# Kernel tuning notes

Hardware: AMD Instinct MI355X
Metric: run time of the kernel (lower is better)

Reference implementation:

```python
import jax, jax.numpy as jnp
import numpy as np

NUM_HEADS = 32  # head_dim = input_dim // num_heads = 32 == C (forced by matmul contraction)


def setup_inputs() -> dict:
    key = jax.random.key(0)
    ks = jax.random.split(key, 8)
    B, C, D3, H1 = 16, 32, 1, 32
    input_dim = 1024  # == C**2, forced by the final view(B, C, H1, W1)
    s = 0.02
    x1 = jax.random.normal(ks[0], (B, C, D3, H1, input_dim), jnp.float32)
    x2 = jax.random.normal(ks[1], (B, C, D3, H1, input_dim), jnp.float32)
    Wq = jax.random.normal(ks[2], (input_dim, input_dim), jnp.float32) * s
    bq = jax.random.normal(ks[3], (input_dim,), jnp.float32) * s
    Wk = jax.random.normal(ks[4], (input_dim, input_dim), jnp.float32) * s
    bk = jax.random.normal(ks[5], (input_dim,), jnp.float32) * s
    Wv = jax.random.normal(ks[6], (input_dim, input_dim), jnp.float32) * s
    bv = jax.random.normal(ks[7], (input_dim,), jnp.float32) * s
    return {"x1": x1, "x2": x2, "Wq": Wq, "bq": bq, "Wk": Wk, "bk": bk, "Wv": Wv, "bv": bv}


def reference(x1, x2, Wq, bq, Wk, bk, Wv, bv):
    B, C, _, H1, W1 = x1.shape  # W1 == input_dim (Linear acts on last dim)
    nh = NUM_HEADS
    hd = W1 // nh
    # Linear projections on the last axis (torch Linear: x @ W.T + b)
    q = (x1 @ Wq.T + bq).reshape(B, C, nh, hd, -1).transpose(0, 2, 4, 3, 1)  # (B, nh, L1, hd, C)
    k = (x2 @ Wk.T + bk).reshape(B, C, nh, hd, -1)                            # (B, C, nh, hd, L2)
    v = (x2 @ Wv.T + bv).reshape(B, C, nh, hd, -1)                            # (B, C, nh, hd, L2)
    # Broadcasted batched matmul: contracts q's trailing C axis with k's hd axis (C == hd).
    energy = jnp.matmul(q, k)                      # (B, C, L1, hd, L2)
    attention = jax.nn.softmax(energy, axis=-1)    # softmax over L2
    # Contracts v's L2 axis with attention's hd axis (L2 == hd).
    out = jnp.matmul(v, attention)                 # (B, C, L1, hd, L2)
    out = out.transpose(0, 2, 4, 3, 1).reshape(B, C, H1, W1)
    return out
```

## Files before the change

kernel.cpp:

```cpp
#include <hip/hip_runtime.h>
#include <cstdint>

typedef __bf16 bf16x8 __attribute__((ext_vector_type(8)));
typedef float f32x4 __attribute__((ext_vector_type(4)));
typedef unsigned short us8 __attribute__((ext_vector_type(8)));

__device__ __forceinline__ unsigned short f2bf(float f) {
  union { float f; uint32_t u; } c; c.f = f;
  uint32_t u = c.u + 0x7FFFu + ((c.u >> 16) & 1u);
  return (unsigned short)(u >> 16);
}

__global__ __launch_bounds__(256) void cvt5(
    const float* __restrict__ x1, const float* __restrict__ x2,
    const float* __restrict__ Wq, const float* __restrict__ Wk, const float* __restrict__ Wv,
    unsigned short* __restrict__ xb1, unsigned short* __restrict__ xb2,
    unsigned short* __restrict__ wb) {
  int z = blockIdx.y;
  const float* src; unsigned short* dst; int n4;
  if (z == 0)      { src = x1; dst = xb1;            n4 = 16777216 / 4; }
  else if (z == 1) { src = x2; dst = xb2;            n4 = 16777216 / 4; }
  else if (z == 2) { src = Wq; dst = wb;             n4 = 1048576 / 4; }
  else if (z == 3) { src = Wk; dst = wb + 1048576;   n4 = 1048576 / 4; }
  else             { src = Wv; dst = wb + 2*1048576; n4 = 1048576 / 4; }
  for (int i = blockIdx.x * 256 + threadIdx.x; i < n4; i += gridDim.x * 256) {
    float4 v = ((const float4*)src)[i];
    ushort4 o;
    o.x = f2bf(v.x); o.y = f2bf(v.y); o.z = f2bf(v.z); o.w = f2bf(v.w);
    ((ushort4*)dst)[i] = o;
  }
}

__device__ __forceinline__ void stage_half(const unsigned short* __restrict__ g,
                                           unsigned short* l, int wv, int rl, int cg) {
#pragma unroll
  for (int ld = 0; ld < 2; ++ld) {
    const int chunk = wv * 2 + ld;
    const unsigned short* gp = g + (chunk * 8 + rl) * 1024 + cg * 8;
    unsigned short* lp = l + chunk * 512;
    __builtin_amdgcn_global_load_lds((const __attribute__((address_space(1))) void*)gp,
                                     (__attribute__((address_space(3))) void*)lp,
                                     16, 0, 0);
  }
}

__global__ __launch_bounds__(512) void gemm_qkv(
    const unsigned short* __restrict__ xb1, const unsigned short* __restrict__ xb2,
    const unsigned short* __restrict__ wb,
    const float* __restrict__ bq, const float* __restrict__ bk, const float* __restrict__ bv,
    unsigned short* __restrict__ qkv) {
  __shared__ __attribute__((aligned(16))) unsigned short sm[65536];
  unsigned short* lA0 = sm;
  unsigned short* lB0 = sm + 16384;
  unsigned short* lA1 = sm + 32768;
  unsigned short* lB1 = sm + 49152;

  const int id = blockIdx.x;
  const int swz = (id & 7) * 96 + (id >> 3);
  const int z = swz >> 8;
  const int rem = swz & 255;
  const int mb = rem >> 2;
  const int nb = rem & 3;
  const int m0 = mb * 256;
  const int n0 = nb * 256;

  const unsigned short* Ag = (z == 0) ? xb1 : xb2;
  const unsigned short* Wg = wb + z * 1048576;
  const float* bias = (z == 0) ? bq : (z == 1 ? bk : bv);
  unsigned short* C = qkv + z * 16777216;

  const int tid = threadIdx.x;
  const int lane = tid & 63;
  const int wv = tid >> 6;
  const int wm = wv >> 2;
  const int wn = wv & 3;
  const int mr = lane & 15;
  const int quad = lane >> 4;

  const int rl = lane >> 3;
  const int cg = (lane & 7) ^ rl;

  const int sg0 = ((quad) ^ (mr & 7)) * 8;
  const int sg1 = ((4 + quad) ^ (mr & 7)) * 8;
  const int arow = (wm * 128 + mr) * 64;
  const int brow = (wn * 64 + mr) * 64;

  f32x4 acc[8][4];
#pragma unroll
  for (int i = 0; i < 8; ++i)
#pragma unroll
    for (int j = 0; j < 4; ++j) acc[i][j] = (f32x4){0.f, 0.f, 0.f, 0.f};

  bf16x8 af[4][2], bfr[4][2];

  auto STA = [&](unsigned short* dst, int kt) {
    const unsigned short* g = Ag + m0 * 1024 + kt * 64;
    stage_half(g, dst, wv, rl, cg);
    stage_half(g + 128 * 1024, dst + 8192, wv, rl, cg);
  };
  auto STB = [&](unsigned short* dst, int kt) {
    const unsigned short* g = Wg + n0 * 1024 + kt * 64;
    stage_half(g, dst, wv, rl, cg);
    stage_half(g + 128 * 1024, dst + 8192, wv, rl, cg);
  };
  auto RDA = [&](const unsigned short* lA, int ib) {
#pragma unroll
    for (int i = 0; i < 4; ++i) {
      af[i][0] = *(const bf16x8*)(lA + arow + (ib + i) * 1024 + sg0);
      af[i][1] = *(const bf16x8*)(lA + arow + (ib + i) * 1024 + sg1);
    }
  };
  auto RDB = [&](const unsigned short* lB, int jb) {
#pragma unroll
    for (int j = 0; j < 2; ++j) {
      bfr[jb + j][0] = *(const bf16x8*)(lB + brow + (jb + j) * 1024 + sg0);
      bfr[jb + j][1] = *(const bf16x8*)(lB + brow + (jb + j) * 1024 + sg1);
    }
  };
  auto MF = [&](int ib, int jb) {
#pragma unroll
    for (int i = 0; i < 4; ++i)
#pragma unroll
      for (int j = 0; j < 2; ++j)
#pragma unroll
        for (int h = 0; h < 2; ++h)
          acc[ib + i][jb + j] = __builtin_amdgcn_mfma_f32_16x16x32_bf16(
              af[i][h], bfr[jb + j][h], acc[ib + i][jb + j], 0, 0, 0);
  };

  STA(lA0, 0);
  STB(lB0, 0);
  STA(lA1, 1);
  asm volatile("s_waitcnt vmcnt(4)" ::: "memory");
  __builtin_amdgcn_s_barrier();

#pragma unroll 1
  for (int t = 0; t < 8; ++t) {
    const bool lastt = (t == 7);
    RDA(lA0, 0); RDB(lB0, 0);
    STB(lB1, 2 * t + 1);
    __builtin_amdgcn_s_barrier();
    __builtin_amdgcn_s_setprio(1); MF(0, 0); __builtin_amdgcn_s_setprio(0);
    __builtin_amdgcn_s_barrier();
    RDB(lB0, 2);
    __builtin_amdgcn_s_barrier();
    __builtin_amdgcn_s_setprio(1); MF(0, 2); __builtin_amdgcn_s_setprio(0);
    __builtin_amdgcn_s_barrier();
    RDA(lA0, 4);
    __builtin_amdgcn_s_barrier();
    __builtin_amdgcn_s_setprio(1); MF(4, 0); __builtin_amdgcn_s_setprio(0);
    __builtin_amdgcn_s_barrier();
    if (!lastt) STA(lA0, 2 * t + 2);
    __builtin_amdgcn_s_barrier();
    __builtin_amdgcn_s_setprio(1); MF(4, 2); __builtin_amdgcn_s_setprio(0);
    if (lastt) { asm volatile("s_waitcnt vmcnt(0)" ::: "memory"); }
    else       { asm volatile("s_waitcnt vmcnt(4)" ::: "memory"); }
    __builtin_amdgcn_s_barrier();
    RDA(lA1, 0); RDB(lB1, 0);
    if (!lastt) STB(lB0, 2 * t + 2);
    __builtin_amdgcn_s_barrier();
    __builtin_amdgcn_s_setprio(1); MF(0, 0); __builtin_amdgcn_s_setprio(0);
    __builtin_amdgcn_s_barrier();
    RDB(lB1, 2);
    __builtin_amdgcn_s_barrier();
    __builtin_amdgcn_s_setprio(1); MF(0, 2); __builtin_amdgcn_s_setprio(0);
    __builtin_amdgcn_s_barrier();
    RDA(lA1, 4);
    __builtin_amdgcn_s_barrier();
    __builtin_amdgcn_s_setprio(1); MF(4, 0); __builtin_amdgcn_s_setprio(0);
    __builtin_amdgcn_s_barrier();
    if (!lastt) STA(lA1, 2 * t + 3);
    __builtin_amdgcn_s_barrier();
    __builtin_amdgcn_s_setprio(1); MF(4, 2); __builtin_amdgcn_s_setprio(0);
    if (!lastt) { asm volatile("s_waitcnt vmcnt(4)" ::: "memory"); }
    __builtin_amdgcn_s_barrier();
  }

  {
    unsigned short* strip = sm + wv * 8192;
    float bb[4];
#pragma unroll
    for (int j = 0; j < 4; ++j) bb[j] = bias[n0 + wn * 64 + j * 16 + mr];
#pragma unroll
    for (int i = 0; i < 8; ++i)
#pragma unroll
      for (int j = 0; j < 4; ++j)
#pragma unroll
        for (int r = 0; r < 4; ++r) {
          int row = i * 16 + quad * 4 + r;
          int byteoff = (row * 128 + j * 32 + mr * 2) ^ (((row >> 2) & 3) << 5);
          *(unsigned short*)((char*)strip + byteoff) = f2bf(acc[i][j][r] + bb[j]);
        }
    const int r8 = lane >> 3, c8 = lane & 7;
#pragma unroll
    for (int it = 0; it < 16; ++it) {
      int row = it * 8 + r8;
      int byteoff = (row * 128 + c8 * 16) ^ (((row >> 2) & 3) << 5);
      uint4 vv = *(const uint4*)((const char*)strip + byteoff);
      *(uint4*)(C + (m0 + wm * 128 + row) * 1024 + n0 + wn * 64 + c8 * 8) = vv;
    }
  }
}

__global__ __launch_bounds__(256) void attn(const unsigned short* __restrict__ qkv,
                                            float* __restrict__ obuf) {
  const unsigned short* qbuf = qkv;
  const unsigned short* kbuf = qkv + 16777216;
  const unsigned short* vbuf = qkv + 2 * 16777216;
  __shared__ __attribute__((aligned(16))) unsigned short qs[8192];
  __shared__ __attribute__((aligned(16))) unsigned short ks[4][1024];
  __shared__ __attribute__((aligned(16))) unsigned short vs[4][1024];
  __shared__ __attribute__((aligned(16))) unsigned short ats[4][1024];
  const int id = blockIdx.x;
  const int xcd = id & 7;
  const int pos = id >> 3;
  const int y0 = (pos & 3) * 8;
  const int bx = (pos >> 2) * 8 + xcd;
  const int b = bx >> 5;
  const int x = bx & 31;
  const int lane = threadIdx.x & 63;
  const int wv = threadIdx.x >> 6;
  const int mr = lane & 15, quad = lane >> 4;

#pragma unroll
  for (int it = 0; it < 4; ++it) {
    int c = threadIdx.x + 256 * it;
    int t = c >> 5, m = c & 31;
    const uint4* src = (const uint4*)(qbuf + ((b * 1024 + t * 32 + x) * 1024 + m * 32 + y0));
    ((uint4*)qs)[c] = *src;
  }
  __syncthreads();

  for (int s = 0; s < 2; ++s) {
    int y = y0 + wv * 2 + s;
    int dy = wv * 2 + s;
    const unsigned short* krow = kbuf + ((b * 32 + x) * 32 + y) * 1024;
    const unsigned short* vrow = vbuf + ((b * 32 + x) * 32 + y) * 1024;
    ((uint4*)ks[wv])[lane] = ((const uint4*)krow)[lane];
    ((uint4*)ks[wv])[64 + lane] = ((const uint4*)krow)[64 + lane];
    ((uint4*)vs[wv])[lane] = ((const uint4*)vrow)[lane];
    ((uint4*)vs[wv])[64 + lane] = ((const uint4*)vrow)[64 + lane];

    bf16x8 qa[2], kb[2];
#pragma unroll
    for (int mt = 0; mt < 2; ++mt) {
      us8 tmp;
#pragma unroll
      for (int jj = 0; jj < 8; ++jj)
        tmp[jj] = qs[((quad * 8 + jj) * 32 + mt * 16 + mr) * 8 + dy];
      qa[mt] = __builtin_bit_cast(bf16x8, tmp);
    }
#pragma unroll
    for (int lt = 0; lt < 2; ++lt) {
      us8 tmp;
#pragma unroll
      for (int jj = 0; jj < 8; ++jj)
        tmp[jj] = ks[wv][(quad * 8 + jj) * 32 + lt * 16 + mr];
      kb[lt] = __builtin_bit_cast(bf16x8, tmp);
    }
    f32x4 e[2][2];
#pragma unroll
    for (int mt = 0; mt < 2; ++mt)
#pragma unroll
      for (int lt = 0; lt < 2; ++lt) {
        f32x4 zz = (f32x4){0.f, 0.f, 0.f, 0.f};
        e[mt][lt] = __builtin_amdgcn_mfma_f32_16x16x32_bf16(qa[mt], kb[lt], zz, 0, 0, 0);
      }

#pragma unroll
    for (int mt = 0; mt < 2; ++mt)
#pragma unroll
      for (int r = 0; r < 4; ++r) {
        float v0 = e[mt][0][r], v1 = e[mt][1][r];
        float mx = fmaxf(v0, v1);
#pragma unroll
        for (int off = 1; off < 16; off <<= 1) mx = fmaxf(mx, __shfl_xor(mx, off));
        float p0 = __expf(v0 - mx), p1 = __expf(v1 - mx);
        float sm = p0 + p1;
#pragma unroll
        for (int off = 1; off < 16; off <<= 1) sm += __shfl_xor(sm, off);
        float inv = 1.0f / sm;
        p0 *= inv; p1 *= inv;
        int trow = mt * 16 + quad * 4 + r;
        ats[wv][trow * 32 + mr] = f2bf(p0);
        ats[wv][trow * 32 + 16 + mr] = f2bf(p1);
      }

    bf16x8 va[2], pb[2];
#pragma unroll
    for (int i = 0; i < 2; ++i)
      va[i] = *(const bf16x8*)(&vs[wv][(i * 16 + mr) * 32 + quad * 8]);
#pragma unroll
    for (int lt = 0; lt < 2; ++lt) {
      us8 tmp;
#pragma unroll
      for (int jj = 0; jj < 8; ++jj)
        tmp[jj] = ats[wv][(quad * 8 + jj) * 32 + lt * 16 + mr];
      pb[lt] = __builtin_bit_cast(bf16x8, tmp);
    }
    f32x4 o[2][2];
#pragma unroll
    for (int i = 0; i < 2; ++i)
#pragma unroll
      for (int lt = 0; lt < 2; ++lt) {
        f32x4 zz = (f32x4){0.f, 0.f, 0.f, 0.f};
        o[i][lt] = __builtin_amdgcn_mfma_f32_16x16x32_bf16(va[i], pb[lt], zz, 0, 0, 0);
      }

    float* orow = obuf + ((b * 32 + x) * 32 + y) * 1024;
#pragma unroll
    for (int i = 0; i < 2; ++i)
#pragma unroll
      for (int lt = 0; lt < 2; ++lt)
#pragma unroll
        for (int r = 0; r < 4; ++r)
          orow[(i * 16 + quad * 4 + r) * 32 + lt * 16 + mr] = o[i][lt][r];
  }
}

__global__ __launch_bounds__(256) void transpose2(const float* __restrict__ obuf,
                                                  float* __restrict__ out) {
  __shared__ float t[2][32][36];
  const int y = blockIdx.y, b = blockIdx.z;
  const int r = threadIdx.x >> 3;
  const int cg = threadIdx.x & 7;
  for (int mi = 0; mi < 8; ++mi) {
    int m = blockIdx.x * 8 + mi;
    int buf = mi & 1;
    float4 v = *(const float4*)(obuf + ((b * 32 + r) * 32 + y) * 1024 + m * 32 + cg * 4);
    *(float4*)&t[buf][r][cg * 4] = v;
    __syncthreads();
    float4 w;
    w.x = t[buf][cg * 4 + 0][r];
    w.y = t[buf][cg * 4 + 1][r];
    w.z = t[buf][cg * 4 + 2][r];
    w.w = t[buf][cg * 4 + 3][r];
    *(float4*)(out + ((b * 32 + y) * 32 + r) * 1024 + m * 32 + cg * 4) = w;
  }
}

extern "C" void kernel_launch(void* const* d_in, const int* in_sizes, int n_in,
                              void* d_out, int out_size, void* d_ws, size_t ws_size,
                              hipStream_t stream) {
  const float* x1 = (const float*)d_in[0];
  const float* x2 = (const float*)d_in[1];
  const float* Wq = (const float*)d_in[2];
  const float* bq = (const float*)d_in[3];
  const float* Wk = (const float*)d_in[4];
  const float* bk = (const float*)d_in[5];
  const float* Wv = (const float*)d_in[6];
  const float* bv = (const float*)d_in[7];
  float* out = (float*)d_out;

  char* ws = (char*)d_ws;
  unsigned short* xb1 = (unsigned short*)ws;
  unsigned short* xb2 = xb1 + 16777216;
  unsigned short* wb = xb2 + 16777216;
  unsigned short* qkv = wb + 3 * 1048576;
  float* obuf = (float*)ws;

  cvt5<<<dim3(2048, 5), 256, 0, stream>>>(x1, x2, Wq, Wk, Wv, xb1, xb2, wb);
  gemm_qkv<<<dim3(768), 512, 0, stream>>>(xb1, xb2, wb, bq, bk, bv, qkv);
  attn<<<dim3(2048), 256, 0, stream>>>(qkv, obuf);
  transpose2<<<dim3(4, 32, 16), 256, 0, stream>>>(obuf, out);
}
```

Baseline: 338.7 us.

## Store attention intermediate as bf16 and transpose softmax tile layout in LDS

New measurement: 330.2 us. 2.5% less time.

```diff
diff --git a/kernel.cpp b/kernel.cpp
--- a/kernel.cpp
+++ b/kernel.cpp
@@ -9,6 +9,9 @@
   union { float f; uint32_t u; } c; c.f = f;
   uint32_t u = c.u + 0x7FFFu + ((c.u >> 16) & 1u);
   return (unsigned short)(u >> 16);
+}
+__device__ __forceinline__ float bf2f(unsigned short u) {
+  union { uint32_t u; float f; } c; c.u = ((uint32_t)u) << 16; return c.f;
 }
 
 __global__ __launch_bounds__(256) void cvt5(
@@ -203,14 +206,15 @@
 }
 
 __global__ __launch_bounds__(256) void attn(const unsigned short* __restrict__ qkv,
-                                            float* __restrict__ obuf) {
+                                            unsigned short* __restrict__ obuf) {
   const unsigned short* qbuf = qkv;
   const unsigned short* kbuf = qkv + 16777216;
   const unsigned short* vbuf = qkv + 2 * 16777216;
   __shared__ __attribute__((aligned(16))) unsigned short qs[8192];
   __shared__ __attribute__((aligned(16))) unsigned short ks[4][1024];
   __shared__ __attribute__((aligned(16))) unsigned short vs[4][1024];
-  __shared__ __attribute__((aligned(16))) unsigned short ats[4][1024];
+  __shared__ __attribute__((aligned(16))) unsigned short ats[4][1280];
+  __shared__ __attribute__((aligned(16))) unsigned short obb[4][1024];
   const int id = blockIdx.x;
   const int xcd = id & 7;
   const int pos = id >> 3;
@@ -282,8 +286,8 @@
         float inv = 1.0f / sm;
         p0 *= inv; p1 *= inv;
         int trow = mt * 16 + quad * 4 + r;
-        ats[wv][trow * 32 + mr] = f2bf(p0);
-        ats[wv][trow * 32 + 16 + mr] = f2bf(p1);
+        ats[wv][mr * 40 + trow] = f2bf(p0);
+        ats[wv][(16 + mr) * 40 + trow] = f2bf(p1);
       }
 
     bf16x8 va[2], pb[2];
@@ -291,13 +295,8 @@
     for (int i = 0; i < 2; ++i)
       va[i] = *(const bf16x8*)(&vs[wv][(i * 16 + mr) * 32 + quad * 8]);
 #pragma unroll
-    for (int lt = 0; lt < 2; ++lt) {
-      us8 tmp;
-#pragma unroll
-      for (int jj = 0; jj < 8; ++jj)
-        tmp[jj] = ats[wv][(quad * 8 + jj) * 32 + lt * 16 + mr];
-      pb[lt] = __builtin_bit_cast(bf16x8, tmp);
-    }
+    for (int lt = 0; lt < 2; ++lt)
+      pb[lt] = *(const bf16x8*)(&ats[wv][(lt * 16 + mr) * 40 + quad * 8]);
     f32x4 o[2][2];
 #pragma unroll
     for (int i = 0; i < 2; ++i)
@@ -307,18 +306,21 @@
         o[i][lt] = __builtin_amdgcn_mfma_f32_16x16x32_bf16(va[i], pb[lt], zz, 0, 0, 0);
       }
 
-    float* orow = obuf + ((b * 32 + x) * 32 + y) * 1024;
 #pragma unroll
     for (int i = 0; i < 2; ++i)
 #pragma unroll
       for (int lt = 0; lt < 2; ++lt)
 #pragma unroll
         for (int r = 0; r < 4; ++r)
-          orow[(i * 16 + quad * 4 + r) * 32 + lt * 16 + mr] = o[i][lt][r];
-  }
-}
-
-__global__ __launch_bounds__(256) void transpose2(const float* __restrict__ obuf,
+          obb[wv][(i * 16 + quad * 4 + r) * 32 + lt * 16 + mr] = f2bf(o[i][lt][r]);
+    unsigned short* orow = obuf + ((b * 32 + x) * 32 + y) * 1024;
+#pragma unroll
+    for (int h = 0; h < 2; ++h)
+      *(uint4*)(orow + h * 512 + lane * 8) = *(const uint4*)(&obb[wv][h * 512 + lane * 8]);
+  }
+}
+
+__global__ __launch_bounds__(256) void transpose2(const unsigned short* __restrict__ obuf,
                                                   float* __restrict__ out) {
   __shared__ float t[2][32][36];
   const int y = blockIdx.y, b = blockIdx.z;
@@ -327,8 +329,11 @@
   for (int mi = 0; mi < 8; ++mi) {
     int m = blockIdx.x * 8 + mi;
     int buf = mi & 1;
-    float4 v = *(const float4*)(obuf + ((b * 32 + r) * 32 + y) * 1024 + m * 32 + cg * 4);
-    *(float4*)&t[buf][r][cg * 4] = v;
+    ushort4 v = *(const ushort4*)(obuf + ((b * 32 + r) * 32 + y) * 1024 + m * 32 + cg * 4);
+    t[buf][r][cg * 4 + 0] = bf2f(v.x);
+    t[buf][r][cg * 4 + 1] = bf2f(v.y);
+    t[buf][r][cg * 4 + 2] = bf2f(v.z);
+    t[buf][r][cg * 4 + 3] = bf2f(v.w);
     __syncthreads();
     float4 w;
     w.x = t[buf][cg * 4 + 0][r];
@@ -357,10 +362,10 @@
   unsigned short* xb2 = xb1 + 16777216;
   unsigned short* wb = xb2 + 16777216;
   unsigned short* qkv = wb + 3 * 1048576;
-  float* obuf = (float*)ws;
+  unsigned short* obuf16 = (unsigned short*)ws;
 
   cvt5<<<dim3(2048, 5), 256, 0, stream>>>(x1, x2, Wq, Wk, Wv, xb1, xb2, wb);
   gemm_qkv<<<dim3(768), 512, 0, stream>>>(xb1, xb2, wb, bq, bk, bv, qkv);
-  attn<<<dim3(2048), 256, 0, stream>>>(qkv, obuf);
-  transpose2<<<dim3(4, 32, 16), 256, 0, stream>>>(obuf, out);
-}
+  attn<<<dim3(2048), 256, 0, stream>>>(qkv, obuf16);
+  transpose2<<<dim3(4, 32, 16), 256, 0, stream>>>(obuf16, out);
+}
```
